# Kernel optimization log

Measured on AMD Instinct MI355X. Metric: run time of the kernel, lower is better.

Reference implementation:

```python
import math
import jax, jax.numpy as jnp
import numpy as np

B, L, D_MODEL, H = 8, 4096, 1024, 16
D_HEAD = D_MODEL // H
FACTOR = 5
U = max(int(math.ceil(math.log(L))) * FACTOR, 1)  # 45 = sample_k = n_top


def setup_inputs() -> dict:
    key = jax.random.key(0)
    ks = jax.random.split(key, 12)
    s = 0.02
    return {
        "Q": jax.random.normal(ks[0], (B, L, D_MODEL), jnp.float32),
        "K": jax.random.normal(ks[1], (B, L, D_MODEL), jnp.float32),
        "V": jax.random.normal(ks[2], (B, L, D_MODEL), jnp.float32),
        "Wq": jax.random.normal(ks[3], (D_MODEL, D_MODEL), jnp.float32) * s,
        "bq": jnp.zeros((D_MODEL,), jnp.float32),
        "Wk": jax.random.normal(ks[4], (D_MODEL, D_MODEL), jnp.float32) * s,
        "bk": jnp.zeros((D_MODEL,), jnp.float32),
        "Wv": jax.random.normal(ks[5], (D_MODEL, D_MODEL), jnp.float32) * s,
        "bv": jnp.zeros((D_MODEL,), jnp.float32),
        "Wo": jax.random.normal(ks[6], (D_MODEL, D_MODEL), jnp.float32) * s,
        "bo": jnp.zeros((D_MODEL,), jnp.float32),
        "index_sample": jax.random.randint(ks[7], (U,), 0, L, dtype=jnp.int32),
    }


def reference(Q, K, V, Wq, bq, Wk, bk, Wv, bv, Wo, bo, index_sample):
    scale = 1.0 / math.sqrt(D_HEAD)
    # projections (torch Linear: x @ W.T + b), split into heads -> [B,H,L,D]
    q = (Q @ Wq.T + bq).reshape(B, L, H, D_HEAD).transpose(0, 2, 1, 3)
    k = (K @ Wk.T + bk).reshape(B, L, H, D_HEAD).transpose(0, 2, 1, 3)
    v = (V @ Wv.T + bv).reshape(B, L, H, D_HEAD).transpose(0, 2, 1, 3)
    # _prob_QK: sample U keys, score every query against them
    k_samp = k[:, :, index_sample, :]                        # [B,H,U,D]
    qk_samp = jnp.einsum('bhqd,bhsd->bhqs', q, k_samp)       # [B,H,L,U]
    M = qk_samp.max(-1) - qk_samp.mean(-1)                   # [B,H,L] max-mean sparsity metric
    _, m_top = jax.lax.top_k(M, U)                           # [B,H,U] top query indices
    # gather top queries, reduced attention over ALL keys
    q_red = jnp.take_along_axis(q, m_top[..., None], axis=2)  # [B,H,U,D]
    scores = jnp.einsum('bhud,bhkd->bhuk', q_red, k) * scale  # [B,H,U,L]
    attn = jax.nn.softmax(scores, axis=-1)
    ctx = jnp.einsum('bhuk,bhkd->bhud', attn, v)              # [B,H,U,D]
    ctx_mean = ctx.mean(axis=2)                               # [B,H,D]
    ctx_flat = ctx_mean.transpose(0, 2, 1).reshape(B, D_MODEL)  # transpose(1,2).view(B,-1)
    return ctx_flat @ Wo.T + bo                               # [B, d_model]
```

## Files before the change

### kernel.cpp

```cpp
#include <hip/hip_runtime.h>
#include <stdint.h>

#define B_ 8
#define L_ 4096
#define DM_ 1024
#define H_ 16
#define DH_ 64
#define U_ 45
#define BH_ 128
#define CHUNKS_ 2

typedef unsigned short u16;
typedef unsigned int u32;
typedef __attribute__((ext_vector_type(8))) short short8;
typedef __attribute__((ext_vector_type(4))) float f32x4;

__device__ __forceinline__ u16 f2bf_rne(float x){
  u32 u = __float_as_uint(x);
  return (u16)((u + 0x7FFFu + ((u >> 16) & 1u)) >> 16);
}
__device__ __forceinline__ float bf2f(u16 v){ return __uint_as_float(((u32)v) << 16); }

__device__ __forceinline__ void gload_lds16(const void* g, void* l){
  auto gp = (const __attribute__((address_space(1))) u32*)(uintptr_t)g;
  auto lp = (__attribute__((address_space(3))) u32*)(u32)(uintptr_t)l;
  __builtin_amdgcn_global_load_lds(gp, lp, 16, 0, 0);
}

__device__ __forceinline__ void split1(float x, u16& h, u16& l){
  h = f2bf_rne(x);
  l = f2bf_rne(x - bf2f(h));
}

__global__ void prep_w(const float* __restrict__ Wq, const float* __restrict__ Wk,
                       const float* __restrict__ Wv,
                       u16* __restrict__ WQH, u16* __restrict__ WQL,
                       u16* __restrict__ WKH, u16* __restrict__ WKL,
                       u16* __restrict__ WVH){
  const int i = (blockIdx.x * 256 + threadIdx.x) * 4;
  float4 a; ushort4 h, l;
  a = *(const float4*)(Wq + i);
  split1(a.x, h.x, l.x); split1(a.y, h.y, l.y); split1(a.z, h.z, l.z); split1(a.w, h.w, l.w);
  *(ushort4*)(WQH + i) = h; *(ushort4*)(WQL + i) = l;
  a = *(const float4*)(Wk + i);
  split1(a.x, h.x, l.x); split1(a.y, h.y, l.y); split1(a.z, h.z, l.z); split1(a.w, h.w, l.w);
  *(ushort4*)(WKH + i) = h; *(ushort4*)(WKL + i) = l;
  a = *(const float4*)(Wv + i);
  split1(a.x, h.x, l.x); split1(a.y, h.y, l.y); split1(a.z, h.z, l.z); split1(a.w, h.w, l.w);
  *(ushort4*)(WVH + i) = h;
}

__global__ void gather_rows(const float* __restrict__ K, const int* __restrict__ IDX,
                            float* __restrict__ GATH){
  const int blk = blockIdx.x;
  const int b = blk / 48, u = blk % 48;
  const int t = threadIdx.x;
  float4 v = make_float4(0.f, 0.f, 0.f, 0.f);
  if (u < U_){
    const int row = IDX[u];
    v = ((const float4*)(K + ((size_t)b * L_ + row) * DM_))[t];
  }
  ((float4*)(GATH + ((size_t)(b * 48 + u)) * DM_))[t] = v;
}

template<int PASSES, int OUTMODE, bool WITHM>
__launch_bounds__(256, 2)
__global__ void gemm_proj(const float* __restrict__ A, const u16* __restrict__ BHp,
                          const u16* __restrict__ BLp, const float* __restrict__ bias,
                          void* __restrict__ outp,
                          const u16* __restrict__ KSH, const u16* __restrict__ KSL,
                          float* __restrict__ MBUF){
  constexpr int LDSB = WITHM ? 69632 : (PASSES == 3 ? 65536 : 49152);
  __shared__ __attribute__((aligned(16))) char smem[LDSB];
  float* As = (float*)smem;
  u16* Bhs = (u16*)(smem + 32768);
  u16* Bls = (u16*)(smem + 49152);

  const int n0 = blockIdx.x * 128;
  const int m0 = blockIdx.y * 128;
  const int t = threadIdx.x;
  const int w = t >> 6, lane = t & 63;
  const int wr = w >> 1, wc = w & 1;
  const int m16 = lane & 15, q4 = lane >> 4;

  f32x4 acc[4][4];
#pragma unroll
  for (int i = 0; i < 4; i++)
#pragma unroll
    for (int j = 0; j < 4; j++) acc[i][j] = (f32x4){0.f, 0.f, 0.f, 0.f};

  const int arow = lane >> 4;
  const int acN  = lane & 15;
  const int brow = lane >> 3;
  const int bcN  = lane & 7;

  for (int kt = 0; kt < 16; kt++){
    const int k0 = kt * 64;
#pragma unroll
    for (int ii = 0; ii < 8; ii++){
      const int nn = w * 8 + ii;
      const int rl = 4 * nn + arow;
      const int c2 = acN ^ (rl & 15);
      const float* gp = A + (size_t)(m0 + rl) * DM_ + (k0 + c2 * 4);
      gload_lds16(gp, As + nn * 256);
    }
#pragma unroll
    for (int ii = 0; ii < 4; ii++){
      const int nn = w * 4 + ii;
      const int rb = 8 * nn + brow;
      const int cb = bcN ^ (brow & 7);
      const size_t go = (size_t)(n0 + rb) * DM_ + (k0 + cb * 8);
      gload_lds16(BHp + go, Bhs + nn * 512);
      if constexpr (PASSES == 3) gload_lds16(BLp + go, Bls + nn * 512);
    }
    __syncthreads();

#pragma unroll
    for (int ks = 0; ks < 2; ks++){
      const int gc0 = ks * 8 + q4 * 2;
      short8 ah[4], al[4];
#pragma unroll
      for (int i = 0; i < 4; i++){
        const float* base = As + (wr * 64 + i * 16 + m16) * 64;
        const f32x4 xlo = *(const f32x4*)(base + (gc0 ^ m16) * 4);
        const f32x4 xhi = *(const f32x4*)(base + ((gc0 + 1) ^ m16) * 4);
        float xx[8] = {xlo[0], xlo[1], xlo[2], xlo[3], xhi[0], xhi[1], xhi[2], xhi[3]};
        short8 h, l;
#pragma unroll
        for (int c = 0; c < 8; c++){
          const u32 ub = __float_as_uint(xx[c]);
          h[c] = (short)(ub >> 16);
          if constexpr (PASSES == 3){
            const float r = xx[c] - __uint_as_float(ub & 0xFFFF0000u);
            l[c] = (short)(__float_as_uint(r) >> 16);
          }
        }
        ah[i] = h;
        if constexpr (PASSES == 3) al[i] = l;
      }
      const int gcb = ks * 4 + q4;
      short8 bh8[4], bl8[4];
#pragma unroll
      for (int j = 0; j < 4; j++){
        const int rowb = wc * 64 + j * 16 + m16;
        const int pos = gcb ^ (m16 & 7);
        bh8[j] = *(const short8*)(Bhs + rowb * 64 + pos * 8);
        if constexpr (PASSES == 3) bl8[j] = *(const short8*)(Bls + rowb * 64 + pos * 8);
      }
#pragma unroll
      for (int i = 0; i < 4; i++)
#pragma unroll
        for (int j = 0; j < 4; j++){
          acc[i][j] = __builtin_amdgcn_mfma_f32_16x16x32_bf16(ah[i], bh8[j], acc[i][j], 0, 0, 0);
          if constexpr (PASSES == 3){
            acc[i][j] = __builtin_amdgcn_mfma_f32_16x16x32_bf16(ah[i], bl8[j], acc[i][j], 0, 0, 0);
            acc[i][j] = __builtin_amdgcn_mfma_f32_16x16x32_bf16(al[i], bh8[j], acc[i][j], 0, 0, 0);
          }
        }
    }
    __syncthreads();
  }

  float* mt = (float*)smem + w * (64 * 68);
  if constexpr (OUTMODE == 3){
    u16* tb = (u16*)smem;
    const int b = m0 >> 12;
    const int l0 = m0 & 4095;
#pragma unroll
    for (int p = 0; p < 2; p++){
      if (wc == p){
#pragma unroll
        for (int j = 0; j < 4; j++){
          const int cl = j * 16 + m16;
          const float bv = bias[n0 + p * 64 + cl];
#pragma unroll
          for (int i = 0; i < 4; i++){
#pragma unroll
            for (int r = 0; r < 4; r++){
              const int gl = wr * 64 + i * 16 + q4 * 4 + r;
              tb[cl * 136 + gl] = f2bf_rne(acc[i][j][r] + bv);
            }
          }
        }
      }
      __syncthreads();
      {
        const int cl = t >> 2;
        const int c = n0 + p * 64 + cl;
        const int h = c >> 6, d = c & 63;
        u16* dst = (u16*)outp + ((size_t)((b * H_ + h) * DH_ + d)) * L_ + l0;
#pragma unroll
        for (int k = 0; k < 4; k++){
          const int ch = (t & 3) + k * 4;
          *(short8*)(dst + ch * 8) = *(const short8*)(tb + cl * 136 + ch * 8);
        }
      }
      __syncthreads();
    }
  } else {
#pragma unroll
    for (int j = 0; j < 4; j++){
      const int c = n0 + wc * 64 + j * 16 + m16;
      const float bv = bias[c];
#pragma unroll
      for (int i = 0; i < 4; i++){
        const int mb = m0 + wr * 64 + i * 16 + q4 * 4;
#pragma unroll
        for (int r = 0; r < 4; r++){
          const int g = mb + r;
          const float val = acc[i][j][r] + bv;
          if constexpr (OUTMODE == 2){
            ((float*)outp)[(size_t)g * DM_ + c] = val;
          } else {
            const int b = g >> 12, l2 = g & 4095;
            const int h = c >> 6, d = c & 63;
            const size_t oi = (((size_t)(b * H_ + h)) * L_ + l2) * DH_ + d;
            if constexpr (OUTMODE == 0) ((float*)outp)[oi] = val;
            else ((u16*)outp)[oi] = (u16)(__float_as_uint(val) >> 16);
          }
          if constexpr (WITHM)
            mt[(i * 16 + q4 * 4 + r) * 68 + (j * 16 + m16)] = val;
        }
      }
    }
  }

  if constexpr (WITHM){
    const int bb = m0 >> 12;
    const int head = (n0 >> 6) + wc;
    const int bh2 = bb * H_ + head;
    f32x4 S[4][3];
#pragma unroll
    for (int im = 0; im < 4; im++)
#pragma unroll
      for (int jt = 0; jt < 3; jt++) S[im][jt] = (f32x4){0.f, 0.f, 0.f, 0.f};
#pragma unroll
    for (int ks = 0; ks < 2; ks++){
      short8 kh3[3], kl3[3];
#pragma unroll
      for (int jt = 0; jt < 3; jt++){
        const size_t ko = ((size_t)bh2 * 48 + jt * 16 + m16) * 64 + ks * 32 + q4 * 8;
        kh3[jt] = *(const short8*)(KSH + ko);
        kl3[jt] = *(const short8*)(KSL + ko);
      }
#pragma unroll
      for (int im = 0; im < 4; im++){
        const float* ap = mt + (im * 16 + m16) * 68 + ks * 32 + q4 * 8;
        const f32x4 xlo = *(const f32x4*)ap;
        const f32x4 xhi = *(const f32x4*)(ap + 4);
        float xx[8] = {xlo[0], xlo[1], xlo[2], xlo[3], xhi[0], xhi[1], xhi[2], xhi[3]};
        short8 qh, ql;
#pragma unroll
        for (int c = 0; c < 8; c++){
          const u32 ub = __float_as_uint(xx[c]);
          qh[c] = (short)(ub >> 16);
          const float r = xx[c] - __uint_as_float(ub & 0xFFFF0000u);
          ql[c] = (short)(__float_as_uint(r) >> 16);
        }
#pragma unroll
        for (int jt = 0; jt < 3; jt++){
          S[im][jt] = __builtin_amdgcn_mfma_f32_16x16x32_bf16(qh, kh3[jt], S[im][jt], 0, 0, 0);
          S[im][jt] = __builtin_amdgcn_mfma_f32_16x16x32_bf16(qh, kl3[jt], S[im][jt], 0, 0, 0);
          S[im][jt] = __builtin_amdgcn_mfma_f32_16x16x32_bf16(ql, kh3[jt], S[im][jt], 0, 0, 0);
        }
      }
    }
#pragma unroll
    for (int im = 0; im < 4; im++)
#pragma unroll
      for (int r = 0; r < 4; r++){
        float mx = -1e30f, sm = 0.f;
#pragma unroll
        for (int jt = 0; jt < 3; jt++){
          const bool ok = (jt < 2) || (m16 < 13);
          const float v = S[im][jt][r];
          if (ok){ mx = fmaxf(mx, v); sm += v; }
        }
#pragma unroll
        for (int off = 1; off < 16; off <<= 1){
          mx = fmaxf(mx, __shfl_xor(mx, off));
          sm += __shfl_xor(sm, off);
        }
        if (m16 == 0){
          const int l2 = (m0 & 4095) + wr * 64 + im * 16 + q4 * 4 + r;
          MBUF[(size_t)bh2 * L_ + l2] = mx - sm * (1.0f / 45.0f);
        }
      }
  }
}

__global__ void ksprep(const float* __restrict__ KSAMP, u16* __restrict__ KSH,
                       u16* __restrict__ KSL){
  const int bh = blockIdx.x;
  const int b = bh >> 4, h = bh & 15;
  const int t = threadIdx.x;
  for (int i = t; i < 48 * 64; i += 256){
    const int u = i >> 6, d = i & 63;
    const float v = (u < U_) ? KSAMP[(size_t)(b * 48 + u) * DM_ + h * DH_ + d] : 0.f;
    u16 hh, ll; split1(v, hh, ll);
    KSH[(size_t)bh * 48 * 64 + i] = hh;
    KSL[(size_t)bh * 48 * 64 + i] = ll;
  }
}

__global__ void topk45(const float* __restrict__ MBUF, int* __restrict__ MTOP){
  const int bh = blockIdx.x;
  const int t = threadIdx.x, w = t >> 6, lane = t & 63;
  __shared__ float Mv[L_];
  __shared__ float rv[4];
  __shared__ int ri[4];
  for (int i = t; i < L_; i += 256) Mv[i] = MBUF[(size_t)bh * L_ + i];
  __syncthreads();
  for (int it = 0; it < U_; it++){
    float bv = -1e30f; int bi = 0;
#pragma unroll
    for (int c = 0; c < 16; c++){
      const int idx = c * 256 + t;
      const float v = Mv[idx];
      if (v > bv || (v == bv && idx < bi)){ bv = v; bi = idx; }
    }
#pragma unroll
    for (int off = 1; off < 64; off <<= 1){
      const float ov = __shfl_xor(bv, off);
      const int oi = __shfl_xor(bi, off);
      if (ov > bv || (ov == bv && oi < bi)){ bv = ov; bi = oi; }
    }
    if (lane == 0){ rv[w] = bv; ri[w] = bi; }
    __syncthreads();
    if (t == 0){
      float fb = rv[0]; int fi = ri[0];
#pragma unroll
      for (int s = 1; s < 4; s++)
        if (rv[s] > fb || (rv[s] == fb && ri[s] < fi)){ fb = rv[s]; fi = ri[s]; }
      MTOP[bh * U_ + it] = fi;
      Mv[fi] = -1e30f;
    }
    __syncthreads();
  }
}

__launch_bounds__(256, 2)
__global__ void attn_fused(const float* __restrict__ QF, const u16* __restrict__ KB,
                           const u16* __restrict__ VT, const int* __restrict__ MTOP,
                           float* __restrict__ MLP, float* __restrict__ CTXP){
  const int bh = blockIdx.x;
  const int chunk = blockIdx.y;
  const int t = threadIdx.x, w = t >> 6, lane = t & 63;
  const int m16 = lane & 15, q4 = lane >> 4;

  __shared__ __attribute__((aligned(16))) float qs[48 * 68];
  __shared__ __attribute__((aligned(16))) u16 ps[4][48 * 72];

  for (int i = t; i < 48 * 64; i += 256){
    const int r = i >> 6, d = i & 63;
    float v = 0.f;
    if (r < U_) v = QF[((size_t)bh * L_ + MTOP[bh * U_ + r]) * DH_ + d] * 0.125f;
    qs[r * 68 + d] = v;
  }
  __syncthreads();

  short8 qh[3][2], ql[3][2];
#pragma unroll
  for (int i = 0; i < 3; i++)
#pragma unroll
    for (int ks = 0; ks < 2; ks++){
      const float* ap = qs + (i * 16 + m16) * 68 + ks * 32 + q4 * 8;
      const f32x4 xlo = *(const f32x4*)ap;
      const f32x4 xhi = *(const f32x4*)(ap + 4);
      float xx[8] = {xlo[0], xlo[1], xlo[2], xlo[3], xhi[0], xhi[1], xhi[2], xhi[3]};
      short8 h, l;
#pragma unroll
      for (int c = 0; c < 8; c++){
        const u32 ub = __float_as_uint(xx[c]);
        h[c] = (short)(ub >> 16);
        const float r = xx[c] - __uint_as_float(ub & 0xFFFF0000u);
        l[c] = (short)(__float_as_uint(r) >> 16);
      }
      qh[i][ks] = h; ql[i][ks] = l;
    }

  float m_run[3][4], l_run[3][4];
  f32x4 O[3][4];
#pragma unroll
  for (int i = 0; i < 3; i++)
#pragma unroll
    for (int r = 0; r < 4; r++){
      m_run[i][r] = -1e30f; l_run[i][r] = 0.f;
      O[i][r] = (f32x4){0.f, 0.f, 0.f, 0.f};
    }

  const u16* kb = KB + (size_t)bh * L_ * DH_;
  const u16* vt = VT + (size_t)bh * DH_ * L_;
  const int TPW = L_ / (CHUNKS_ * 4 * 64);
  u16* pw = ps[w];

  for (int tt = 0; tt < TPW; tt++){
    const int t0 = ((chunk * 4 + w) * TPW + tt) * 64;
    f32x4 S[3][4];
#pragma unroll
    for (int i = 0; i < 3; i++)
#pragma unroll
      for (int jt = 0; jt < 4; jt++) S[i][jt] = (f32x4){0.f, 0.f, 0.f, 0.f};
#pragma unroll
    for (int ks = 0; ks < 2; ks++){
      short8 kf[4];
#pragma unroll
      for (int jt = 0; jt < 4; jt++)
        kf[jt] = *(const short8*)(kb + (size_t)(t0 + jt * 16 + m16) * DH_ + ks * 32 + q4 * 8);
#pragma unroll
      for (int i = 0; i < 3; i++)
#pragma unroll
        for (int jt = 0; jt < 4; jt++){
          S[i][jt] = __builtin_amdgcn_mfma_f32_16x16x32_bf16(qh[i][ks], kf[jt], S[i][jt], 0, 0, 0);
          S[i][jt] = __builtin_amdgcn_mfma_f32_16x16x32_bf16(ql[i][ks], kf[jt], S[i][jt], 0, 0, 0);
        }
    }
#pragma unroll
    for (int i = 0; i < 3; i++){
      float mnew[4], alpha[4], psum[4];
#pragma unroll
      for (int r = 0; r < 4; r++){
        float mx = fmaxf(fmaxf(S[i][0][r], S[i][1][r]), fmaxf(S[i][2][r], S[i][3][r]));
        mx = fmaxf(mx, __shfl_xor(mx, 1));
        mx = fmaxf(mx, __shfl_xor(mx, 2));
        mx = fmaxf(mx, __shfl_xor(mx, 4));
        mx = fmaxf(mx, __shfl_xor(mx, 8));
        mnew[r] = fmaxf(m_run[i][r], mx);
        alpha[r] = __expf(m_run[i][r] - mnew[r]);
        m_run[i][r] = mnew[r];
        l_run[i][r] *= alpha[r];
        psum[r] = 0.f;
      }
#pragma unroll
      for (int jo = 0; jo < 4; jo++)
#pragma unroll
        for (int r = 0; r < 4; r++) O[i][jo][r] *= alpha[r];
#pragma unroll
      for (int jt = 0; jt < 4; jt++)
#pragma unroll
        for (int r = 0; r < 4; r++){
          const float pv = __expf(S[i][jt][r] - mnew[r]);
          const u16 pq = f2bf_rne(pv);
          psum[r] += bf2f(pq);
          pw[(i * 16 + q4 * 4 + r) * 72 + jt * 16 + m16] = pq;
        }
#pragma unroll
      for (int r = 0; r < 4; r++){
        float s = psum[r];
        s += __shfl_xor(s, 1); s += __shfl_xor(s, 2);
        s += __shfl_xor(s, 4); s += __shfl_xor(s, 8);
        l_run[i][r] += s;
      }
    }
#pragma unroll
    for (int ks = 0; ks < 2; ks++){
      short8 pa[3], vf[4];
#pragma unroll
      for (int i = 0; i < 3; i++)
        pa[i] = *(const short8*)(pw + (i * 16 + m16) * 72 + ks * 32 + q4 * 8);
#pragma unroll
      for (int jo = 0; jo < 4; jo++)
        vf[jo] = *(const short8*)(vt + (size_t)(jo * 16 + m16) * L_ + t0 + ks * 32 + q4 * 8);
#pragma unroll
      for (int i = 0; i < 3; i++)
#pragma unroll
        for (int jo = 0; jo < 4; jo++)
          O[i][jo] = __builtin_amdgcn_mfma_f32_16x16x32_bf16(pa[i], vf[jo], O[i][jo], 0, 0, 0);
    }
  }

  const int state = (bh * CHUNKS_ + chunk) * 4 + w;
  float* mlp = MLP + (size_t)state * 48 * 2;
  float* ctxp = CTXP + (size_t)state * 48 * 64;
#pragma unroll
  for (int i = 0; i < 3; i++)
#pragma unroll
    for (int r = 0; r < 4; r++){
      const int row = i * 16 + q4 * 4 + r;
      if (m16 == 0){ mlp[row * 2] = m_run[i][r]; mlp[row * 2 + 1] = l_run[i][r]; }
#pragma unroll
      for (int jo = 0; jo < 4; jo++)
        ctxp[row * 64 + jo * 16 + m16] = O[i][jo][r];
    }
}

__global__ void attn_combine(const float* __restrict__ MLP, const float* __restrict__ CTXP,
                             float* __restrict__ CTXF){
  const int bh = blockIdx.x;
  const int b = bh >> 4, h = bh & 15;
  const int t = threadIdx.x;
  const int col = t & 63, rg = t >> 6;
  const int NS = CHUNKS_ * 4;
  __shared__ float ml[8 * 48 * 2];
  __shared__ float red[4][64];
  for (int i = t; i < NS * 48 * 2; i += 256) ml[i] = MLP[(size_t)bh * NS * 48 * 2 + i];
  __syncthreads();
  float acc = 0.f;
  for (int rr = 0; rr < 12; rr++){
    const int row = rg * 12 + rr;
    if (row >= U_) break;
    float M = -1e30f;
#pragma unroll
    for (int s = 0; s < NS; s++) M = fmaxf(M, ml[s * 96 + row * 2]);
    float num = 0.f, den = 0.f;
#pragma unroll
    for (int s = 0; s < NS; s++){
      const float wgt = __expf(ml[s * 96 + row * 2] - M);
      num += wgt * CTXP[((size_t)bh * NS + s) * 48 * 64 + row * 64 + col];
      den += wgt * ml[s * 96 + row * 2 + 1];
    }
    acc += num / den;
  }
  red[rg][col] = acc;
  __syncthreads();
  if (t < 64){
    const float v = (red[0][t] + red[1][t] + red[2][t] + red[3][t]) * (1.0f / 45.0f);
    CTXF[b * DM_ + t * H_ + h] = v;
  }
}

__global__ void s4_out(const float* __restrict__ CTXF, const float* __restrict__ Wo,
                       const float* __restrict__ bo, float* __restrict__ out){
  const int jb = blockIdx.x;
  const int b = blockIdx.y;
  const int t = threadIdx.x;
  __shared__ float cx[DM_];
  for (int i = t; i < DM_; i += 256) cx[i] = CTXF[b * DM_ + i];
  __syncthreads();
  const int j = jb * 256 + t;
  const float* wrow = Wo + (size_t)j * DM_;
  float acc = bo[j];
  for (int c = 0; c < 256; c++){
    const float4 wv = *(const float4*)(wrow + c * 4);
    const float4 cv = *(const float4*)(cx + c * 4);
    acc += wv.x * cv.x + wv.y * cv.y + wv.z * cv.z + wv.w * cv.w;
  }
  out[b * DM_ + j] = acc;
}

extern "C" void kernel_launch(void* const* d_in, const int* in_sizes, int n_in,
                              void* d_out, int out_size, void* d_ws, size_t ws_size,
                              hipStream_t stream){
  const float* Q  = (const float*)d_in[0];
  const float* K  = (const float*)d_in[1];
  const float* V  = (const float*)d_in[2];
  const float* Wq = (const float*)d_in[3];
  const float* bq = (const float*)d_in[4];
  const float* Wk = (const float*)d_in[5];
  const float* bk = (const float*)d_in[6];
  const float* Wv = (const float*)d_in[7];
  const float* bv = (const float*)d_in[8];
  const float* Wo = (const float*)d_in[9];
  const float* bo = (const float*)d_in[10];
  const int* IDX  = (const int*)d_in[11];
  float* out = (float*)d_out;

  char* p = (char*)d_ws;
  auto alloc = [&](size_t bytes) -> char* {
    char* r = p; p += (bytes + 255) & ~(size_t)255; return r;
  };
  u16*  WQH  = (u16*)alloc((size_t)DM_ * DM_ * 2);
  u16*  WQL  = (u16*)alloc((size_t)DM_ * DM_ * 2);
  u16*  WKH  = (u16*)alloc((size_t)DM_ * DM_ * 2);
  u16*  WKL  = (u16*)alloc((size_t)DM_ * DM_ * 2);
  u16*  WVH  = (u16*)alloc((size_t)DM_ * DM_ * 2);
  float* QF  = (float*)alloc((size_t)BH_ * L_ * DH_ * 4);
  u16*  KB   = (u16*)alloc((size_t)BH_ * L_ * DH_ * 2);
  u16*  VT   = (u16*)alloc((size_t)BH_ * DH_ * L_ * 2);
  float* GATH = (float*)alloc((size_t)B_ * 48 * DM_ * 4);
  float* KSAMP= (float*)alloc((size_t)B_ * 48 * DM_ * 4);
  u16*  KSH  = (u16*)alloc((size_t)BH_ * 48 * DH_ * 2);
  u16*  KSL  = (u16*)alloc((size_t)BH_ * 48 * DH_ * 2);
  float* MBUF = (float*)alloc((size_t)BH_ * L_ * 4);
  int*   MTOP = (int*)alloc((size_t)BH_ * U_ * 4);
  float* MLP  = (float*)alloc((size_t)BH_ * CHUNKS_ * 4 * 48 * 2 * 4);
  float* CTXP = (float*)alloc((size_t)BH_ * CHUNKS_ * 4 * 48 * 64 * 4);
  float* CTXF = (float*)alloc((size_t)B_ * DM_ * 4);

  prep_w<<<dim3(1024), dim3(256), 0, stream>>>(Wq, Wk, Wv, WQH, WQL, WKH, WKL, WVH);
  gather_rows<<<dim3(B_ * 48), dim3(256), 0, stream>>>(K, IDX, GATH);
  gemm_proj<3, 2, false><<<dim3(8, 3), dim3(256), 0, stream>>>(
      GATH, WKH, WKL, bk, (void*)KSAMP, nullptr, nullptr, nullptr);
  ksprep<<<dim3(BH_), dim3(256), 0, stream>>>(KSAMP, KSH, KSL);
  gemm_proj<3, 0, true><<<dim3(8, 256), dim3(256), 0, stream>>>(
      Q, WQH, WQL, bq, (void*)QF, KSH, KSL, MBUF);
  gemm_proj<1, 1, false><<<dim3(8, 256), dim3(256), 0, stream>>>(
      K, WKH, nullptr, bk, (void*)KB, nullptr, nullptr, nullptr);
  gemm_proj<1, 3, false><<<dim3(8, 256), dim3(256), 0, stream>>>(
      V, WVH, nullptr, bv, (void*)VT, nullptr, nullptr, nullptr);
  topk45<<<dim3(BH_), dim3(256), 0, stream>>>(MBUF, MTOP);
  attn_fused<<<dim3(BH_, CHUNKS_), dim3(256), 0, stream>>>(QF, KB, VT, MTOP, MLP, CTXP);
  attn_combine<<<dim3(BH_), dim3(256), 0, stream>>>(MLP, CTXP, CTXF);
  s4_out<<<dim3(4, 8), dim3(256), 0, stream>>>(CTXF, Wo, bo, out);
}
```

Measured before the change: 997.5 us.

## Pre-split Q into bf16 hi/lo, drop full QF write, recompute top queries

Result: slower. 1.062 ms (+6.5%).

```diff
diff --git a/kernel.cpp b/kernel.cpp
--- a/kernel.cpp
+++ b/kernel.cpp
@@ -8,7 +8,7 @@
 #define DH_ 64
 #define U_ 45
 #define BH_ 128
-#define CHUNKS_ 2
+#define CHUNKS_ 4
 
 typedef unsigned short u16;
 typedef unsigned int u32;
@@ -50,8 +50,17 @@
   *(ushort4*)(WVH + i) = h;
 }
 
+__global__ void splitq(const float* __restrict__ Q, u16* __restrict__ QH,
+                       u16* __restrict__ QL){
+  const int i = (blockIdx.x * 256 + threadIdx.x) * 4;
+  const float4 a = *(const float4*)(Q + i);
+  ushort4 h, l;
+  split1(a.x, h.x, l.x); split1(a.y, h.y, l.y); split1(a.z, h.z, l.z); split1(a.w, h.w, l.w);
+  *(ushort4*)(QH + i) = h; *(ushort4*)(QL + i) = l;
+}
+
 __global__ void gather_rows(const float* __restrict__ K, const int* __restrict__ IDX,
-                            float* __restrict__ GATH){
+                            u16* __restrict__ GATHH, u16* __restrict__ GATHL){
   const int blk = blockIdx.x;
   const int b = blk / 48, u = blk % 48;
   const int t = threadIdx.x;
@@ -60,19 +69,23 @@
     const int row = IDX[u];
     v = ((const float4*)(K + ((size_t)b * L_ + row) * DM_))[t];
   }
-  ((float4*)(GATH + ((size_t)(b * 48 + u)) * DM_))[t] = v;
-}
-
-template<int PASSES, int OUTMODE, bool WITHM>
+  ushort4 h, l;
+  split1(v.x, h.x, l.x); split1(v.y, h.y, l.y); split1(v.z, h.z, l.z); split1(v.w, h.w, l.w);
+  ((ushort4*)(GATHH + ((size_t)(b * 48 + u)) * DM_))[t] = h;
+  ((ushort4*)(GATHL + ((size_t)(b * 48 + u)) * DM_))[t] = l;
+}
+
+template<int OUTMODE, bool WITHM>
 __launch_bounds__(256, 2)
-__global__ void gemm_proj(const float* __restrict__ A, const u16* __restrict__ BHp,
-                          const u16* __restrict__ BLp, const float* __restrict__ bias,
-                          void* __restrict__ outp,
-                          const u16* __restrict__ KSH, const u16* __restrict__ KSL,
-                          float* __restrict__ MBUF){
-  constexpr int LDSB = WITHM ? 69632 : (PASSES == 3 ? 65536 : 49152);
+__global__ void gemm_asplit(const u16* __restrict__ AH, const u16* __restrict__ AL,
+                            const u16* __restrict__ BHp, const u16* __restrict__ BLp,
+                            const float* __restrict__ bias, void* __restrict__ outp,
+                            const u16* __restrict__ KSH, const u16* __restrict__ KSL,
+                            float* __restrict__ MBUF){
+  constexpr int LDSB = WITHM ? 69632 : 65536;
   __shared__ __attribute__((aligned(16))) char smem[LDSB];
-  float* As = (float*)smem;
+  u16* Ahs = (u16*)smem;
+  u16* Als = (u16*)(smem + 16384);
   u16* Bhs = (u16*)(smem + 32768);
   u16* Bls = (u16*)(smem + 49152);
 
@@ -89,6 +102,164 @@
 #pragma unroll
     for (int j = 0; j < 4; j++) acc[i][j] = (f32x4){0.f, 0.f, 0.f, 0.f};
 
+  const int brow = lane >> 3;
+  const int bcN  = lane & 7;
+
+  for (int kt = 0; kt < 16; kt++){
+    const int k0 = kt * 64;
+#pragma unroll
+    for (int ii = 0; ii < 4; ii++){
+      const int nn = w * 4 + ii;
+      const int rb = 8 * nn + brow;
+      const int cb = bcN ^ (brow & 7);
+      const size_t goA = (size_t)(m0 + rb) * DM_ + (k0 + cb * 8);
+      const size_t goB = (size_t)(n0 + rb) * DM_ + (k0 + cb * 8);
+      gload_lds16(AH + goA, Ahs + nn * 512);
+      gload_lds16(AL + goA, Als + nn * 512);
+      gload_lds16(BHp + goB, Bhs + nn * 512);
+      gload_lds16(BLp + goB, Bls + nn * 512);
+    }
+    __syncthreads();
+
+#pragma unroll
+    for (int ks = 0; ks < 2; ks++){
+      const int gcb = ks * 4 + q4;
+      const int posm = (gcb ^ (m16 & 7)) * 8;
+      short8 ah[4], al[4], bh8[4], bl8[4];
+#pragma unroll
+      for (int i = 0; i < 4; i++){
+        const int rowa = (wr * 64 + i * 16 + m16) * 64;
+        ah[i] = *(const short8*)(Ahs + rowa + posm);
+        al[i] = *(const short8*)(Als + rowa + posm);
+      }
+#pragma unroll
+      for (int j = 0; j < 4; j++){
+        const int rowb = (wc * 64 + j * 16 + m16) * 64;
+        bh8[j] = *(const short8*)(Bhs + rowb + posm);
+        bl8[j] = *(const short8*)(Bls + rowb + posm);
+      }
+#pragma unroll
+      for (int i = 0; i < 4; i++)
+#pragma unroll
+        for (int j = 0; j < 4; j++){
+          acc[i][j] = __builtin_amdgcn_mfma_f32_16x16x32_bf16(ah[i], bh8[j], acc[i][j], 0, 0, 0);
+          acc[i][j] = __builtin_amdgcn_mfma_f32_16x16x32_bf16(ah[i], bl8[j], acc[i][j], 0, 0, 0);
+          acc[i][j] = __builtin_amdgcn_mfma_f32_16x16x32_bf16(al[i], bh8[j], acc[i][j], 0, 0, 0);
+        }
+    }
+    __syncthreads();
+  }
+
+  if constexpr (OUTMODE == 2){
+#pragma unroll
+    for (int j = 0; j < 4; j++){
+      const int c = n0 + wc * 64 + j * 16 + m16;
+      const float bv = bias[c];
+#pragma unroll
+      for (int i = 0; i < 4; i++){
+        const int mb = m0 + wr * 64 + i * 16 + q4 * 4;
+#pragma unroll
+        for (int r = 0; r < 4; r++)
+          ((float*)outp)[(size_t)(mb + r) * DM_ + c] = acc[i][j][r] + bv;
+      }
+    }
+  }
+
+  if constexpr (WITHM){
+    float* mt = (float*)smem + w * (64 * 68);
+#pragma unroll
+    for (int j = 0; j < 4; j++){
+      const float bv = bias[n0 + wc * 64 + j * 16 + m16];
+#pragma unroll
+      for (int i = 0; i < 4; i++)
+#pragma unroll
+        for (int r = 0; r < 4; r++)
+          mt[(i * 16 + q4 * 4 + r) * 68 + (j * 16 + m16)] = acc[i][j][r] + bv;
+    }
+    const int bb = m0 >> 12;
+    const int head = (n0 >> 6) + wc;
+    const int bh2 = bb * H_ + head;
+    f32x4 S[4][3];
+#pragma unroll
+    for (int im = 0; im < 4; im++)
+#pragma unroll
+      for (int jt = 0; jt < 3; jt++) S[im][jt] = (f32x4){0.f, 0.f, 0.f, 0.f};
+#pragma unroll
+    for (int ks = 0; ks < 2; ks++){
+      short8 kh3[3], kl3[3];
+#pragma unroll
+      for (int jt = 0; jt < 3; jt++){
+        const size_t ko = ((size_t)bh2 * 48 + jt * 16 + m16) * 64 + ks * 32 + q4 * 8;
+        kh3[jt] = *(const short8*)(KSH + ko);
+        kl3[jt] = *(const short8*)(KSL + ko);
+      }
+#pragma unroll
+      for (int im = 0; im < 4; im++){
+        const float* ap = mt + (im * 16 + m16) * 68 + ks * 32 + q4 * 8;
+        const f32x4 xlo = *(const f32x4*)ap;
+        const f32x4 xhi = *(const f32x4*)(ap + 4);
+        float xx[8] = {xlo[0], xlo[1], xlo[2], xlo[3], xhi[0], xhi[1], xhi[2], xhi[3]};
+        short8 qh, ql;
+#pragma unroll
+        for (int c = 0; c < 8; c++){
+          const u32 ub = __float_as_uint(xx[c]);
+          qh[c] = (short)(ub >> 16);
+          const float r = xx[c] - __uint_as_float(ub & 0xFFFF0000u);
+          ql[c] = (short)(__float_as_uint(r) >> 16);
+        }
+#pragma unroll
+        for (int jt = 0; jt < 3; jt++){
+          S[im][jt] = __builtin_amdgcn_mfma_f32_16x16x32_bf16(qh, kh3[jt], S[im][jt], 0, 0, 0);
+          S[im][jt] = __builtin_amdgcn_mfma_f32_16x16x32_bf16(qh, kl3[jt], S[im][jt], 0, 0, 0);
+          S[im][jt] = __builtin_amdgcn_mfma_f32_16x16x32_bf16(ql, kh3[jt], S[im][jt], 0, 0, 0);
+        }
+      }
+    }
+#pragma unroll
+    for (int im = 0; im < 4; im++)
+#pragma unroll
+      for (int r = 0; r < 4; r++){
+        float mx = -1e30f, sm = 0.f;
+#pragma unroll
+        for (int jt = 0; jt < 3; jt++){
+          const bool ok = (jt < 2) || (m16 < 13);
+          const float v = S[im][jt][r];
+          if (ok){ mx = fmaxf(mx, v); sm += v; }
+        }
+#pragma unroll
+        for (int off = 1; off < 16; off <<= 1){
+          mx = fmaxf(mx, __shfl_xor(mx, off));
+          sm += __shfl_xor(sm, off);
+        }
+        if (m16 == 0){
+          const int l2 = (m0 & 4095) + wr * 64 + im * 16 + q4 * 4 + r;
+          MBUF[(size_t)bh2 * L_ + l2] = mx - sm * (1.0f / 45.0f);
+        }
+      }
+  }
+}
+
+template<int OUTMODE>
+__launch_bounds__(256, 2)
+__global__ void gemm_f32a(const float* __restrict__ A, const u16* __restrict__ BHp,
+                          const float* __restrict__ bias, void* __restrict__ outp){
+  __shared__ __attribute__((aligned(16))) char smem[49152];
+  float* As = (float*)smem;
+  u16* Bhs = (u16*)(smem + 32768);
+
+  const int n0 = blockIdx.x * 128;
+  const int m0 = blockIdx.y * 128;
+  const int t = threadIdx.x;
+  const int w = t >> 6, lane = t & 63;
+  const int wr = w >> 1, wc = w & 1;
+  const int m16 = lane & 15, q4 = lane >> 4;
+
+  f32x4 acc[4][4];
+#pragma unroll
+  for (int i = 0; i < 4; i++)
+#pragma unroll
+    for (int j = 0; j < 4; j++) acc[i][j] = (f32x4){0.f, 0.f, 0.f, 0.f};
+
   const int arow = lane >> 4;
   const int acN  = lane & 15;
   const int brow = lane >> 3;
@@ -101,67 +272,46 @@
       const int nn = w * 8 + ii;
       const int rl = 4 * nn + arow;
       const int c2 = acN ^ (rl & 15);
-      const float* gp = A + (size_t)(m0 + rl) * DM_ + (k0 + c2 * 4);
-      gload_lds16(gp, As + nn * 256);
+      gload_lds16(A + (size_t)(m0 + rl) * DM_ + (k0 + c2 * 4), As + nn * 256);
     }
 #pragma unroll
     for (int ii = 0; ii < 4; ii++){
       const int nn = w * 4 + ii;
       const int rb = 8 * nn + brow;
       const int cb = bcN ^ (brow & 7);
-      const size_t go = (size_t)(n0 + rb) * DM_ + (k0 + cb * 8);
-      gload_lds16(BHp + go, Bhs + nn * 512);
-      if constexpr (PASSES == 3) gload_lds16(BLp + go, Bls + nn * 512);
+      gload_lds16(BHp + (size_t)(n0 + rb) * DM_ + (k0 + cb * 8), Bhs + nn * 512);
     }
     __syncthreads();
 
 #pragma unroll
     for (int ks = 0; ks < 2; ks++){
       const int gc0 = ks * 8 + q4 * 2;
-      short8 ah[4], al[4];
+      short8 ah[4];
 #pragma unroll
       for (int i = 0; i < 4; i++){
         const float* base = As + (wr * 64 + i * 16 + m16) * 64;
         const f32x4 xlo = *(const f32x4*)(base + (gc0 ^ m16) * 4);
         const f32x4 xhi = *(const f32x4*)(base + ((gc0 + 1) ^ m16) * 4);
         float xx[8] = {xlo[0], xlo[1], xlo[2], xlo[3], xhi[0], xhi[1], xhi[2], xhi[3]};
-        short8 h, l;
-#pragma unroll
-        for (int c = 0; c < 8; c++){
-          const u32 ub = __float_as_uint(xx[c]);
-          h[c] = (short)(ub >> 16);
-          if constexpr (PASSES == 3){
-            const float r = xx[c] - __uint_as_float(ub & 0xFFFF0000u);
-            l[c] = (short)(__float_as_uint(r) >> 16);
-          }
-        }
+        short8 h;
+#pragma unroll
+        for (int c = 0; c < 8; c++) h[c] = (short)(__float_as_uint(xx[c]) >> 16);
         ah[i] = h;
-        if constexpr (PASSES == 3) al[i] = l;
       }
       const int gcb = ks * 4 + q4;
-      short8 bh8[4], bl8[4];
-#pragma unroll
-      for (int j = 0; j < 4; j++){
-        const int rowb = wc * 64 + j * 16 + m16;
-        const int pos = gcb ^ (m16 & 7);
-        bh8[j] = *(const short8*)(Bhs + rowb * 64 + pos * 8);
-        if constexpr (PASSES == 3) bl8[j] = *(const short8*)(Bls + rowb * 64 + pos * 8);
-      }
+      short8 bh8[4];
+#pragma unroll
+      for (int j = 0; j < 4; j++)
+        bh8[j] = *(const short8*)(Bhs + (wc * 64 + j * 16 + m16) * 64 + (gcb ^ (m16 & 7)) * 8);
 #pragma unroll
       for (int i = 0; i < 4; i++)
 #pragma unroll
-        for (int j = 0; j < 4; j++){
+        for (int j = 0; j < 4; j++)
           acc[i][j] = __builtin_amdgcn_mfma_f32_16x16x32_bf16(ah[i], bh8[j], acc[i][j], 0, 0, 0);
-          if constexpr (PASSES == 3){
-            acc[i][j] = __builtin_amdgcn_mfma_f32_16x16x32_bf16(ah[i], bl8[j], acc[i][j], 0, 0, 0);
-            acc[i][j] = __builtin_amdgcn_mfma_f32_16x16x32_bf16(al[i], bh8[j], acc[i][j], 0, 0, 0);
-          }
-        }
     }
     __syncthreads();
   }
 
-  float* mt = (float*)smem + w * (64 * 68);
   if constexpr (OUTMODE == 3){
     u16* tb = (u16*)smem;
     const int b = m0 >> 12;
@@ -174,13 +324,12 @@
           const int cl = j * 16 + m16;
           const float bv = bias[n0 + p * 64 + cl];
 #pragma unroll
-          for (int i = 0; i < 4; i++){
+          for (int i = 0; i < 4; i++)
 #pragma unroll
             for (int r = 0; r < 4; r++){
               const int gl = wr * 64 + i * 16 + q4 * 4 + r;
               tb[cl * 136 + gl] = f2bf_rne(acc[i][j][r] + bv);
             }
-          }
         }
       }
       __syncthreads();
@@ -202,90 +351,19 @@
     for (int j = 0; j < 4; j++){
       const int c = n0 + wc * 64 + j * 16 + m16;
       const float bv = bias[c];
+      const int h = c >> 6, d = c & 63;
 #pragma unroll
       for (int i = 0; i < 4; i++){
         const int mb = m0 + wr * 64 + i * 16 + q4 * 4;
 #pragma unroll
         for (int r = 0; r < 4; r++){
           const int g = mb + r;
-          const float val = acc[i][j][r] + bv;
-          if constexpr (OUTMODE == 2){
-            ((float*)outp)[(size_t)g * DM_ + c] = val;
-          } else {
-            const int b = g >> 12, l2 = g & 4095;
-            const int h = c >> 6, d = c & 63;
-            const size_t oi = (((size_t)(b * H_ + h)) * L_ + l2) * DH_ + d;
-            if constexpr (OUTMODE == 0) ((float*)outp)[oi] = val;
-            else ((u16*)outp)[oi] = (u16)(__float_as_uint(val) >> 16);
-          }
-          if constexpr (WITHM)
-            mt[(i * 16 + q4 * 4 + r) * 68 + (j * 16 + m16)] = val;
-        }
-      }
-    }
-  }
-
-  if constexpr (WITHM){
-    const int bb = m0 >> 12;
-    const int head = (n0 >> 6) + wc;
-    const int bh2 = bb * H_ + head;
-    f32x4 S[4][3];
-#pragma unroll
-    for (int im = 0; im < 4; im++)
-#pragma unroll
-      for (int jt = 0; jt < 3; jt++) S[im][jt] = (f32x4){0.f, 0.f, 0.f, 0.f};
-#pragma unroll
-    for (int ks = 0; ks < 2; ks++){
-      short8 kh3[3], kl3[3];
-#pragma unroll
-      for (int jt = 0; jt < 3; jt++){
-        const size_t ko = ((size_t)bh2 * 48 + jt * 16 + m16) * 64 + ks * 32 + q4 * 8;
-        kh3[jt] = *(const short8*)(KSH + ko);
-        kl3[jt] = *(const short8*)(KSL + ko);
-      }
-#pragma unroll
-      for (int im = 0; im < 4; im++){
-        const float* ap = mt + (im * 16 + m16) * 68 + ks * 32 + q4 * 8;
-        const f32x4 xlo = *(const f32x4*)ap;
-        const f32x4 xhi = *(const f32x4*)(ap + 4);
-        float xx[8] = {xlo[0], xlo[1], xlo[2], xlo[3], xhi[0], xhi[1], xhi[2], xhi[3]};
-        short8 qh, ql;
-#pragma unroll
-        for (int c = 0; c < 8; c++){
-          const u32 ub = __float_as_uint(xx[c]);
-          qh[c] = (short)(ub >> 16);
-          const float r = xx[c] - __uint_as_float(ub & 0xFFFF0000u);
-          ql[c] = (short)(__float_as_uint(r) >> 16);
-        }
-#pragma unroll
-        for (int jt = 0; jt < 3; jt++){
-          S[im][jt] = __builtin_amdgcn_mfma_f32_16x16x32_bf16(qh, kh3[jt], S[im][jt], 0, 0, 0);
-          S[im][jt] = __builtin_amdgcn_mfma_f32_16x16x32_bf16(qh, kl3[jt], S[im][jt], 0, 0, 0);
-          S[im][jt] = __builtin_amdgcn_mfma_f32_16x16x32_bf16(ql, kh3[jt], S[im][jt], 0, 0, 0);
-        }
-      }
-    }
-#pragma unroll
-    for (int im = 0; im < 4; im++)
-#pragma unroll
-      for (int r = 0; r < 4; r++){
-        float mx = -1e30f, sm = 0.f;
-#pragma unroll
-        for (int jt = 0; jt < 3; jt++){
-          const bool ok = (jt < 2) || (m16 < 13);
-          const float v = S[im][jt][r];
-          if (ok){ mx = fmaxf(mx, v); sm += v; }
-        }
-#pragma unroll
-        for (int off = 1; off < 16; off <<= 1){
-          mx = fmaxf(mx, __shfl_xor(mx, off));
-          sm += __shfl_xor(sm, off);
-        }
-        if (m16 == 0){
-          const int l2 = (m0 & 4095) + wr * 64 + im * 16 + q4 * 4 + r;
-          MBUF[(size_t)bh2 * L_ + l2] = mx - sm * (1.0f / 45.0f);
-        }
-      }
+          const int b = g >> 12, l2 = g & 4095;
+          ((u16*)outp)[(((size_t)(b * H_ + h)) * L_ + l2) * DH_ + d] =
+              f2bf_rne(acc[i][j][r] + bv);
+        }
+      }
+    }
   }
 }
 
@@ -339,9 +417,56 @@
   }
 }
 
+__global__ void qred_kernel(const u16* __restrict__ QH, const u16* __restrict__ QL,
+                            const u16* __restrict__ WQH, const u16* __restrict__ WQL,
+                            const float* __restrict__ bq, const int* __restrict__ MTOP,
+                            float* __restrict__ QRED){
+  const int bh = blockIdx.x;
+  const int b = bh >> 4, h = bh & 15;
+  const int t = threadIdx.x, w = t >> 6, lane = t & 63;
+  const int m16 = lane & 15, q4 = lane >> 4;
+  __shared__ int rows[48];
+  if (t < 48) rows[t] = (t < U_) ? MTOP[bh * U_ + t] : 0;
+  __syncthreads();
+
+  f32x4 acc[3];
+#pragma unroll
+  for (int i = 0; i < 3; i++) acc[i] = (f32x4){0.f, 0.f, 0.f, 0.f};
+  const int c = h * 64 + w * 16 + m16;
+  const u16* wqh = WQH + (size_t)c * DM_;
+  const u16* wql = WQL + (size_t)c * DM_;
+  size_t abase[3];
+#pragma unroll
+  for (int i = 0; i < 3; i++)
+    abase[i] = ((size_t)b * L_ + rows[i * 16 + m16]) * DM_;
+
+  for (int kk = 0; kk < 32; kk++){
+    const int k = kk * 32 + q4 * 8;
+    const short8 bh8 = *(const short8*)(wqh + k);
+    const short8 bl8 = *(const short8*)(wql + k);
+#pragma unroll
+    for (int i = 0; i < 3; i++){
+      const short8 ah = *(const short8*)(QH + abase[i] + k);
+      const short8 al = *(const short8*)(QL + abase[i] + k);
+      acc[i] = __builtin_amdgcn_mfma_f32_16x16x32_bf16(ah, bh8, acc[i], 0, 0, 0);
+      acc[i] = __builtin_amdgcn_mfma_f32_16x16x32_bf16(ah, bl8, acc[i], 0, 0, 0);
+      acc[i] = __builtin_amdgcn_mfma_f32_16x16x32_bf16(al, bh8, acc[i], 0, 0, 0);
+    }
+  }
+  const float bv = bq[h * 64 + w * 16 + m16];
+#pragma unroll
+  for (int i = 0; i < 3; i++)
+#pragma unroll
+    for (int r = 0; r < 4; r++){
+      const int row = i * 16 + q4 * 4 + r;
+      const float val = (row < U_) ? (acc[i][r] + bv) : 0.f;
+      QRED[((size_t)bh * 48 + row) * 64 + (w * 16 + m16)] = val;
+    }
+}
+
 __launch_bounds__(256, 2)
-__global__ void attn_fused(const float* __restrict__ QF, const u16* __restrict__ KB,
-                           const u16* __restrict__ VT, const int* __restrict__ MTOP,
+__global__ void attn_fused(const float* __restrict__ QRED, const u16* __restrict__ KB,
+                           const u16* __restrict__ VT,
                            float* __restrict__ MLP, float* __restrict__ CTXP){
   const int bh = blockIdx.x;
   const int chunk = blockIdx.y;
@@ -351,12 +476,8 @@
   __shared__ __attribute__((aligned(16))) float qs[48 * 68];
   __shared__ __attribute__((aligned(16))) u16 ps[4][48 * 72];
 
-  for (int i = t; i < 48 * 64; i += 256){
-    const int r = i >> 6, d = i & 63;
-    float v = 0.f;
-    if (r < U_) v = QF[((size_t)bh * L_ + MTOP[bh * U_ + r]) * DH_ + d] * 0.125f;
-    qs[r * 68 + d] = v;
-  }
+  for (int i = t; i < 48 * 64; i += 256)
+    qs[(i >> 6) * 68 + (i & 63)] = QRED[(size_t)bh * 48 * 64 + i] * 0.125f;
   __syncthreads();
 
   short8 qh[3][2], ql[3][2];
@@ -491,7 +612,7 @@
   const int t = threadIdx.x;
   const int col = t & 63, rg = t >> 6;
   const int NS = CHUNKS_ * 4;
-  __shared__ float ml[8 * 48 * 2];
+  __shared__ float ml[CHUNKS_ * 4 * 48 * 2];
   __shared__ float red[4][64];
   for (int i = t; i < NS * 48 * 2; i += 256) ml[i] = MLP[(size_t)bh * NS * 48 * 2 + i];
   __syncthreads();
@@ -564,32 +685,35 @@
   u16*  WKH  = (u16*)alloc((size_t)DM_ * DM_ * 2);
   u16*  WKL  = (u16*)alloc((size_t)DM_ * DM_ * 2);
   u16*  WVH  = (u16*)alloc((size_t)DM_ * DM_ * 2);
-  float* QF  = (float*)alloc((size_t)BH_ * L_ * DH_ * 4);
+  u16*  QH   = (u16*)alloc((size_t)B_ * L_ * DM_ * 2);
+  u16*  QL   = (u16*)alloc((size_t)B_ * L_ * DM_ * 2);
   u16*  KB   = (u16*)alloc((size_t)BH_ * L_ * DH_ * 2);
   u16*  VT   = (u16*)alloc((size_t)BH_ * DH_ * L_ * 2);
-  float* GATH = (float*)alloc((size_t)B_ * 48 * DM_ * 4);
+  u16*  GATHH= (u16*)alloc((size_t)B_ * 48 * DM_ * 2);
+  u16*  GATHL= (u16*)alloc((size_t)B_ * 48 * DM_ * 2);
   float* KSAMP= (float*)alloc((size_t)B_ * 48 * DM_ * 4);
   u16*  KSH  = (u16*)alloc((size_t)BH_ * 48 * DH_ * 2);
   u16*  KSL  = (u16*)alloc((size_t)BH_ * 48 * DH_ * 2);
   float* MBUF = (float*)alloc((size_t)BH_ * L_ * 4);
   int*   MTOP = (int*)alloc((size_t)BH_ * U_ * 4);
+  float* QRED = (float*)alloc((size_t)BH_ * 48 * DH_ * 4);
   float* MLP  = (float*)alloc((size_t)BH_ * CHUNKS_ * 4 * 48 * 2 * 4);
   float* CTXP = (float*)alloc((size_t)BH_ * CHUNKS_ * 4 * 48 * 64 * 4);
   float* CTXF = (float*)alloc((size_t)B_ * DM_ * 4);
 
   prep_w<<<dim3(1024), dim3(256), 0, stream>>>(Wq, Wk, Wv, WQH, WQL, WKH, WKL, WVH);
-  gather_rows<<<dim3(B_ * 48), dim3(256), 0, stream>>>(K, IDX, GATH);
-  gemm_proj<3, 2, false><<<dim3(8, 3), dim3(256), 0, stream>>>(
-      GATH, WKH, WKL, bk, (void*)KSAMP, nullptr, nullptr, nullptr);
+  splitq<<<dim3(B_ * L_ * DM_ / 1024), dim3(256), 0, stream>>>(Q, QH, QL);
+  gather_rows<<<dim3(B_ * 48), dim3(256), 0, stream>>>(K, IDX, GATHH, GATHL);
+  gemm_asplit<2, false><<<dim3(8, 3), dim3(256), 0, stream>>>(
+      GATHH, GATHL, WKH, WKL, bk, (void*)KSAMP, nullptr, nullptr, nullptr);
   ksprep<<<dim3(BH_), dim3(256), 0, stream>>>(KSAMP, KSH, KSL);
-  gemm_proj<3, 0, true><<<dim3(8, 256), dim3(256), 0, stream>>>(
-      Q, WQH, WQL, bq, (void*)QF, KSH, KSL, MBUF);
-  gemm_proj<1, 1, false><<<dim3(8, 256), dim3(256), 0, stream>>>(
-      K, WKH, nullptr, bk, (void*)KB, nullptr, nullptr, nullptr);
-  gemm_proj<1, 3, false><<<dim3(8, 256), dim3(256), 0, stream>>>(
-      V, WVH, nullptr, bv, (void*)VT, nullptr, nullptr, nullptr);
+  gemm_asplit<4, true><<<dim3(8, 256), dim3(256), 0, stream>>>(
+      QH, QL, WQH, WQL, bq, nullptr, KSH, KSL, MBUF);
+  gemm_f32a<1><<<dim3(8, 256), dim3(256), 0, stream>>>(K, WKH, bk, (void*)KB);
+  gemm_f32a<3><<<dim3(8, 256), dim3(256), 0, stream>>>(V, WVH, bv, (void*)VT);
   topk45<<<dim3(BH_), dim3(256), 0, stream>>>(MBUF, MTOP);
-  attn_fused<<<dim3(BH_, CHUNKS_), dim3(256), 0, stream>>>(QF, KB, VT, MTOP, MLP, CTXP);
+  qred_kernel<<<dim3(BH_), dim3(256), 0, stream>>>(QH, QL, WQH, WQL, bq, MTOP, QRED);
+  attn_fused<<<dim3(BH_, CHUNKS_), dim3(256), 0, stream>>>(QRED, KB, VT, MLP, CTXP);
   attn_combine<<<dim3(BH_), dim3(256), 0, stream>>>(MLP, CTXP, CTXF);
   s4_out<<<dim3(4, 8), dim3(256), 0, stream>>>(CTXF, Wo, bo, out);
 }
```
